# Kernel tuning notes

Hardware: AMD Instinct MI355X
Metric: run time of the kernel (lower is better)

The kernel has to match this reference:

```python
import jax, jax.numpy as jnp
import numpy as np

N_NODES = 10000
N_EDGES = 80000
IN_DIM = 512
H1, H2, OUT_DIM = 4096, 1024, 7
NEG_SLOPE = 0.2


def _gat_layer(x, src, dst, W, a_src, a_dst, b, n_nodes):
    # x: [N, F_in] -> h: [N, F_out]
    h = x @ W
    # per-edge attention logits: a_src . h_i + a_dst . h_j (PyG GATConv, heads=1)
    e = jax.nn.leaky_relu((h @ a_src)[src] + (h @ a_dst)[dst], NEG_SLOPE)
    # segment softmax over destination nodes
    m = jax.ops.segment_max(e, dst, num_segments=n_nodes)
    ex = jnp.exp(e - m[dst])
    denom = jax.ops.segment_sum(ex, dst, num_segments=n_nodes)
    alpha = ex / denom[dst]
    # scatter-add weighted messages
    out = jax.ops.segment_sum(alpha[:, None] * h[src], dst, num_segments=n_nodes)
    return out + b


def setup_inputs() -> dict:
    key = jax.random.key(0)
    ks = jax.random.split(key, 16)
    s = 0.05
    inp = {
        "x": jax.random.normal(ks[0], (N_NODES, IN_DIM), dtype=jnp.float32),
        "edge_index": jax.random.randint(ks[1], (2, N_EDGES), 0, N_NODES, dtype=jnp.int32),
        "W1": jax.random.normal(ks[2], (IN_DIM, H1), dtype=jnp.float32) * s,
        "att_src1": jax.random.normal(ks[3], (H1,), dtype=jnp.float32) * s,
        "att_dst1": jax.random.normal(ks[4], (H1,), dtype=jnp.float32) * s,
        "b1": jnp.zeros((H1,), dtype=jnp.float32),
        "W2": jax.random.normal(ks[5], (H1, H2), dtype=jnp.float32) * s,
        "att_src2": jax.random.normal(ks[6], (H2,), dtype=jnp.float32) * s,
        "att_dst2": jax.random.normal(ks[7], (H2,), dtype=jnp.float32) * s,
        "b2": jnp.zeros((H2,), dtype=jnp.float32),
        "W3": jax.random.normal(ks[8], (H2, OUT_DIM), dtype=jnp.float32) * s,
        "att_src3": jax.random.normal(ks[9], (OUT_DIM,), dtype=jnp.float32) * s,
        "att_dst3": jax.random.normal(ks[10], (OUT_DIM,), dtype=jnp.float32) * s,
        "b3": jnp.zeros((OUT_DIM,), dtype=jnp.float32),
    }
    return inp


def reference(x, edge_index, W1, att_src1, att_dst1, b1,
              W2, att_src2, att_dst2, b2,
              W3, att_src3, att_dst3, b3):
    n = x.shape[0]
    loops = jnp.arange(n, dtype=edge_index.dtype)
    src = jnp.concatenate([edge_index[0], loops])  # add_self_loops=True
    dst = jnp.concatenate([edge_index[1], loops])
    h = _gat_layer(x, src, dst, W1, att_src1, att_dst1, b1, n)
    h = jax.nn.relu(h)  # dropout is identity in eval mode
    h = _gat_layer(h, src, dst, W2, att_src2, att_dst2, b2, n)
    h = jax.nn.relu(h)
    h = _gat_layer(h, src, dst, W3, att_src3, att_dst3, b3, n)
    return jax.nn.log_softmax(h, axis=1)
```

## Files before the change

### kernel.cpp

```cpp
#include <hip/hip_runtime.h>
#include <hip/hip_bf16.h>
#include <math.h>

#define NNODES  10000
#define NEDGES  80000
#define NTOT    90000
#define IN_DIM  512
#define H1_DIM  4096
#define H2_DIM  1024
#define ODIM    7
#define MAXDEG  128
#define NEG_SLOPE 0.2f

typedef __hip_bfloat16 bf16;
typedef __attribute__((ext_vector_type(8))) short short8;
typedef __attribute__((ext_vector_type(4))) float f32x4;

__device__ inline float ldf(const float* p, size_t i) { return p[i]; }
__device__ inline float ldf(const bf16* p, size_t i)  { return __bfloat162float(p[i]); }
__device__ inline void  stf(float* p, size_t i, float v) { p[i] = v; }
__device__ inline void  stf(bf16* p, size_t i, float v)  { p[i] = __float2bfloat16(v); }

#define ASYNC_COPY16(lds, g)                                                              \
    __builtin_amdgcn_global_load_lds((const __attribute__((address_space(1))) void*)(g),  \
                                     (__attribute__((address_space(3))) void*)(lds),      \
                                     16, 0, 0)

__global__ void zero_cnt(int* cnt) {
    int i = blockIdx.x * blockDim.x + threadIdx.x;
    if (i < NNODES) cnt[i] = 0;
}

__global__ void build_bucket(const int* __restrict__ ei, int* cnt, int* bucket) {
    int k = blockIdx.x * blockDim.x + threadIdx.x;
    if (k >= NTOT) return;
    int s, d;
    if (k < NEDGES) { s = ei[k]; d = ei[NEDGES + k]; }
    else            { s = k - NEDGES; d = s; }
    int pos = atomicAdd(&cnt[d], 1);
    if (pos < MAXDEG) bucket[d * MAXDEG + pos] = s;
}

__global__ __launch_bounds__(256) void transpose_bf16(const float* __restrict__ W,
                                                      bf16* __restrict__ WT, int R, int C) {
    __shared__ float t[32][33];
    int c0 = blockIdx.x * 32, r0 = blockIdx.y * 32;
    int x = threadIdx.x & 31, y = threadIdx.x >> 5;
    #pragma unroll
    for (int dy = 0; dy < 32; dy += 8)
        t[y + dy][x] = W[(size_t)(r0 + y + dy) * C + c0 + x];
    __syncthreads();
    #pragma unroll
    for (int dy = 0; dy < 32; dy += 8)
        WT[(size_t)(c0 + y + dy) * R + r0 + x] = __float2bfloat16(t[x][y + dy]);
}

__global__ __launch_bounds__(256) void fold_att(const float* __restrict__ W,
                                                const float* __restrict__ a_s,
                                                const float* __restrict__ a_d,
                                                float* __restrict__ w_s,
                                                float* __restrict__ w_d, int C) {
    int r = blockIdx.x;
    const float* row = W + (size_t)r * C;
    float ss = 0.f, sd = 0.f;
    for (int j = threadIdx.x; j < C; j += 256) {
        float w = row[j];
        ss = fmaf(w, a_s[j], ss);
        sd = fmaf(w, a_d[j], sd);
    }
    #pragma unroll
    for (int off = 32; off > 0; off >>= 1) {
        ss += __shfl_down(ss, off);
        sd += __shfl_down(sd, off);
    }
    __shared__ float red[2][4];
    int wave = threadIdx.x >> 6;
    if ((threadIdx.x & 63) == 0) { red[0][wave] = ss; red[1][wave] = sd; }
    __syncthreads();
    if (threadIdx.x == 0) {
        w_s[r] = red[0][0] + red[0][1] + red[0][2] + red[0][3];
        w_d[r] = red[1][0] + red[1][1] + red[1][2] + red[1][3];
    }
}

template<typename IT>
__global__ __launch_bounds__(256) void node_dots_t(const IT* __restrict__ H,
                                                   const float* __restrict__ w_s,
                                                   const float* __restrict__ w_d,
                                                   float* __restrict__ s_src,
                                                   float* __restrict__ s_dst, int F) {
    int n = blockIdx.x;
    const IT* h = H + (size_t)n * F;
    float ss = 0.f, sd = 0.f;
    for (int f = threadIdx.x; f < F; f += 256) {
        float v = ldf(h, f);
        ss = fmaf(v, w_s[f], ss);
        sd = fmaf(v, w_d[f], sd);
    }
    #pragma unroll
    for (int off = 32; off > 0; off >>= 1) {
        ss += __shfl_down(ss, off);
        sd += __shfl_down(sd, off);
    }
    __shared__ float red[2][4];
    int wave = threadIdx.x >> 6;
    if ((threadIdx.x & 63) == 0) { red[0][wave] = ss; red[1][wave] = sd; }
    __syncthreads();
    if (threadIdx.x == 0) {
        s_src[n] = red[0][0] + red[0][1] + red[0][2] + red[0][3];
        s_dst[n] = red[1][0] + red[1][1] + red[1][2] + red[1][3];
    }
}

template<typename IT, typename OT, bool BIASRELU>
__global__ __launch_bounds__(256) void aggregate_t(const IT* __restrict__ H,
                                                   const float* __restrict__ s_src,
                                                   const float* __restrict__ s_dst,
                                                   const int* __restrict__ bucket,
                                                   const int* __restrict__ cnt,
                                                   const float* __restrict__ bias,
                                                   OT* __restrict__ OUT, int F) {
    int n = blockIdx.x;
    int c = min(cnt[n], MAXDEG);
    __shared__ float alpha[MAXDEG];
    __shared__ int   ssrc[MAXDEG];
    if (threadIdx.x < c) {
        int s = bucket[n * MAXDEG + threadIdx.x];
        ssrc[threadIdx.x] = s;
        float e = s_src[s] + s_dst[n];
        alpha[threadIdx.x] = (e > 0.f) ? e : NEG_SLOPE * e;
    }
    __syncthreads();
    if (threadIdx.x == 0) {
        float m = -1e30f;
        for (int j = 0; j < c; ++j) m = fmaxf(m, alpha[j]);
        float s = 0.f;
        for (int j = 0; j < c; ++j) { float ex = __expf(alpha[j] - m); alpha[j] = ex; s += ex; }
        float inv = 1.f / s;
        for (int j = 0; j < c; ++j) alpha[j] *= inv;
    }
    __syncthreads();
    for (int f = threadIdx.x; f < F; f += 256) {
        float acc = 0.f;
        for (int j = 0; j < c; ++j)
            acc = fmaf(alpha[j], ldf(H, (size_t)ssrc[j] * F + f), acc);
        if (BIASRELU) acc = fmaxf(acc + bias[f], 0.f);
        stf(OUT, (size_t)n * F + f, acc);
    }
}

template<bool BIASRELU>
__global__ __launch_bounds__(256) void gemm_mfma(const bf16* __restrict__ A,
                                                 const bf16* __restrict__ BT,
                                                 const float* __restrict__ bias,
                                                 bf16* __restrict__ C,
                                                 int M, int N, int K) {
    __shared__ alignas(16) bf16 As[128][32];
    __shared__ alignas(16) bf16 Bs[128][32];
    const int tid  = threadIdx.x;
    const int wave = tid >> 6;
    const int lane = tid & 63;
    const int row0 = blockIdx.y * 128;
    const int col0 = blockIdx.x * 128;
    const int wr0  = (wave >> 1) * 64;
    const int wc0  = (wave & 1) * 64;

    const int srow  = tid >> 2;
    const int skoff = (tid & 3) * 8;
    const bf16* ag0 = A  + (size_t)min(row0 + srow,      M - 1) * K + skoff;
    const bf16* ag1 = A  + (size_t)min(row0 + 64 + srow, M - 1) * K + skoff;
    const bf16* bg0 = BT + (size_t)(col0 + srow) * K + skoff;
    const bf16* bg1 = BT + (size_t)(col0 + 64 + srow) * K + skoff;
    bf16* la0 = &As[wave * 16][0];
    bf16* la1 = &As[64 + wave * 16][0];
    bf16* lb0 = &Bs[wave * 16][0];
    bf16* lb1 = &Bs[64 + wave * 16][0];

    f32x4 acc[4][4] = {};

    const int fRow  = lane & 15;
    const int fKoff = (lane >> 4) * 8;

    for (int k0 = 0; k0 < K; k0 += 32) {
        ASYNC_COPY16(la0, ag0);
        ASYNC_COPY16(la1, ag1);
        ASYNC_COPY16(lb0, bg0);
        ASYNC_COPY16(lb1, bg1);
        ag0 += 32; ag1 += 32; bg0 += 32; bg1 += 32;
        __syncthreads();
        short8 af[4], bfr[4];
        #pragma unroll
        for (int i = 0; i < 4; ++i)
            af[i] = *(const short8*)&As[wr0 + i * 16 + fRow][fKoff];
        #pragma unroll
        for (int j = 0; j < 4; ++j)
            bfr[j] = *(const short8*)&Bs[wc0 + j * 16 + fRow][fKoff];
        #pragma unroll
        for (int i = 0; i < 4; ++i)
            #pragma unroll
            for (int j = 0; j < 4; ++j)
                acc[i][j] = __builtin_amdgcn_mfma_f32_16x16x32_bf16(af[i], bfr[j], acc[i][j], 0, 0, 0);
        __syncthreads();
    }

    const int crow = (lane >> 4) * 4;
    const int ccol = lane & 15;
    #pragma unroll
    for (int i = 0; i < 4; ++i) {
        #pragma unroll
        for (int r = 0; r < 4; ++r) {
            int gm = row0 + wr0 + i * 16 + crow + r;
            if (gm < M) {
                #pragma unroll
                for (int j = 0; j < 4; ++j) {
                    int gn = col0 + wc0 + j * 16 + ccol;
                    float v = acc[i][j][r];
                    if (BIASRELU) v = fmaxf(v + bias[gn], 0.f);
                    C[(size_t)gm * N + gn] = __float2bfloat16(v);
                }
            }
        }
    }
}

__global__ __launch_bounds__(256) void layer3_proj(const bf16* __restrict__ X,
                                                   const float* __restrict__ W,
                                                   const float* __restrict__ a_src,
                                                   const float* __restrict__ a_dst,
                                                   float* __restrict__ H3,
                                                   float* __restrict__ s_src,
                                                   float* __restrict__ s_dst) {
    int n = blockIdx.x;
    const bf16* x = X + (size_t)n * H2_DIM;
    float acc[ODIM] = {};
    for (int k = threadIdx.x; k < H2_DIM; k += 256) {
        float xv = __bfloat162float(x[k]);
        #pragma unroll
        for (int o = 0; o < ODIM; ++o)
            acc[o] = fmaf(xv, W[k * ODIM + o], acc[o]);
    }
    #pragma unroll
    for (int o = 0; o < ODIM; ++o)
        #pragma unroll
        for (int off = 32; off > 0; off >>= 1)
            acc[o] += __shfl_down(acc[o], off);
    __shared__ float red[4][ODIM];
    int wave = threadIdx.x >> 6;
    if ((threadIdx.x & 63) == 0)
        for (int o = 0; o < ODIM; ++o) red[wave][o] = acc[o];
    __syncthreads();
    if (threadIdx.x == 0) {
        float ss = 0.f, sd = 0.f;
        for (int o = 0; o < ODIM; ++o) {
            float v = red[0][o] + red[1][o] + red[2][o] + red[3][o];
            H3[n * ODIM + o] = v;
            ss = fmaf(v, a_src[o], ss);
            sd = fmaf(v, a_dst[o], sd);
        }
        s_src[n] = ss; s_dst[n] = sd;
    }
}

__global__ __launch_bounds__(128) void aggregate3(const float* __restrict__ H3,
                                                  const float* __restrict__ s_src,
                                                  const float* __restrict__ s_dst,
                                                  const int* __restrict__ bucket,
                                                  const int* __restrict__ cnt,
                                                  const float* __restrict__ b3,
                                                  float* __restrict__ out) {
    int n = blockIdx.x;
    int c = min(cnt[n], MAXDEG);
    __shared__ float alpha[MAXDEG];
    __shared__ int   ssrc[MAXDEG];
    __shared__ float o[ODIM];
    if (threadIdx.x < c) {
        int s = bucket[n * MAXDEG + threadIdx.x];
        ssrc[threadIdx.x] = s;
        float e = s_src[s] + s_dst[n];
        alpha[threadIdx.x] = (e > 0.f) ? e : NEG_SLOPE * e;
    }
    __syncthreads();
    if (threadIdx.x == 0) {
        float m = -1e30f;
        for (int j = 0; j < c; ++j) m = fmaxf(m, alpha[j]);
        float s = 0.f;
        for (int j = 0; j < c; ++j) { float ex = __expf(alpha[j] - m); alpha[j] = ex; s += ex; }
        float inv = 1.f / s;
        for (int j = 0; j < c; ++j) alpha[j] *= inv;
    }
    __syncthreads();
    if (threadIdx.x < ODIM) {
        float acc = 0.f;
        for (int j = 0; j < c; ++j)
            acc = fmaf(alpha[j], H3[ssrc[j] * ODIM + threadIdx.x], acc);
        o[threadIdx.x] = acc + b3[threadIdx.x];
    }
    __syncthreads();
    if (threadIdx.x == 0) {
        float m = o[0];
        for (int k = 1; k < ODIM; ++k) m = fmaxf(m, o[k]);
        float s = 0.f;
        for (int k = 0; k < ODIM; ++k) s += __expf(o[k] - m);
        float lse = m + logf(s);
        for (int k = 0; k < ODIM; ++k) out[n * ODIM + k] = o[k] - lse;
    }
}

extern "C" void kernel_launch(void* const* d_in, const int* in_sizes, int n_in,
                              void* d_out, int out_size, void* d_ws, size_t ws_size,
                              hipStream_t stream) {
    const float* x   = (const float*)d_in[0];
    const int*   ei  = (const int*)  d_in[1];
    const float* W1  = (const float*)d_in[2];
    const float* as1 = (const float*)d_in[3];
    const float* ad1 = (const float*)d_in[4];
    const float* b1  = (const float*)d_in[5];
    const float* W2  = (const float*)d_in[6];
    const float* as2 = (const float*)d_in[7];
    const float* ad2 = (const float*)d_in[8];
    const float* b2  = (const float*)d_in[9];
    const float* W3  = (const float*)d_in[10];
    const float* as3 = (const float*)d_in[11];
    const float* ad3 = (const float*)d_in[12];
    const float* b3  = (const float*)d_in[13];
    float* outp = (float*)d_out;

    char* p = (char*)d_ws;
    bf16*  x2     = (bf16*)p;   p += (size_t)NNODES * H1_DIM * sizeof(bf16);
    bf16*  r2     = (bf16*)p;   p += (size_t)NNODES * H2_DIM * sizeof(bf16);
    bf16*  r3     = (bf16*)p;   p += (size_t)NNODES * H2_DIM * sizeof(bf16);
    bf16*  W2T    = (bf16*)p;   p += (size_t)H2_DIM * H1_DIM * sizeof(bf16);
    float* h3     = (float*)p;  p += (size_t)NNODES * ODIM * sizeof(float);
    float* ssrc   = (float*)p;  p += NNODES * sizeof(float);
    float* sdst   = (float*)p;  p += NNODES * sizeof(float);
    float* w1s    = (float*)p;  p += IN_DIM * sizeof(float);
    float* w1d    = (float*)p;  p += IN_DIM * sizeof(float);
    float* w2s    = (float*)p;  p += H1_DIM * sizeof(float);
    float* w2d    = (float*)p;  p += H1_DIM * sizeof(float);
    int*   cnt    = (int*)p;    p += NNODES * sizeof(int);
    int*   bucket = (int*)p;    p += (size_t)NNODES * MAXDEG * sizeof(int);
    size_t required = (size_t)(p - (char*)d_ws);
    if (ws_size < required) return;

    bf16* aggxb = r2;
    bf16* h2    = r2;
    bf16* W1T   = r3;
    bf16* x3    = r3;

    zero_cnt<<<(NNODES + 255) / 256, 256, 0, stream>>>(cnt);
    build_bucket<<<(NTOT + 255) / 256, 256, 0, stream>>>(ei, cnt, bucket);

    fold_att<<<IN_DIM, 256, 0, stream>>>(W1, as1, ad1, w1s, w1d, H1_DIM);
    node_dots_t<float><<<NNODES, 256, 0, stream>>>(x, w1s, w1d, ssrc, sdst, IN_DIM);
    aggregate_t<float, bf16, false><<<NNODES, 256, 0, stream>>>(x, ssrc, sdst, bucket, cnt, nullptr, aggxb, IN_DIM);
    {
        dim3 tg(H1_DIM / 32, IN_DIM / 32);
        transpose_bf16<<<tg, 256, 0, stream>>>(W1, W1T, IN_DIM, H1_DIM);
        dim3 g(H1_DIM / 128, (NNODES + 127) / 128);
        gemm_mfma<true><<<g, 256, 0, stream>>>(aggxb, W1T, b1, x2, NNODES, H1_DIM, IN_DIM);
    }

    fold_att<<<H1_DIM, 256, 0, stream>>>(W2, as2, ad2, w2s, w2d, H2_DIM);
    node_dots_t<bf16><<<NNODES, 256, 0, stream>>>(x2, w2s, w2d, ssrc, sdst, H1_DIM);
    {
        dim3 tg(H2_DIM / 32, H1_DIM / 32);
        transpose_bf16<<<tg, 256, 0, stream>>>(W2, W2T, H1_DIM, H2_DIM);
        dim3 g(H2_DIM / 128, (NNODES + 127) / 128);
        gemm_mfma<false><<<g, 256, 0, stream>>>(x2, W2T, nullptr, h2, NNODES, H2_DIM, H1_DIM);
    }
    aggregate_t<bf16, bf16, true><<<NNODES, 256, 0, stream>>>(h2, ssrc, sdst, bucket, cnt, b2, x3, H2_DIM);

    layer3_proj<<<NNODES, 256, 0, stream>>>(x3, W3, as3, ad3, h3, ssrc, sdst);
    aggregate3<<<NNODES, 128, 0, stream>>>(h3, ssrc, sdst, bucket, cnt, b3, outp);
}
```

Before: 499.8 us.

## Fuse layer-2 attention dots into GEMM epilogue, vectorize aggregation, retile GEMM

The layer-2 node dot products move into the layer-1 GEMM epilogue as atomic adds, so the 4096-wide activation is no longer re-read in a separate pass. The aggregation kernels are specialized per layer and use vectorized float4/uint4 loads with 128 threads. The GEMM now stages 64 k-values per barrier and uses a 64-column tile for layer 2 to launch more blocks. The zero-count kernel becomes a memset. Risks: atomics make the dot sums order-dependent, and one 64-wide chunk per barrier raises LDS use.

```diff
diff --git a/kernel.cpp b/kernel.cpp
--- a/kernel.cpp
+++ b/kernel.cpp
@@ -18,18 +18,17 @@
 
 __device__ inline float ldf(const float* p, size_t i) { return p[i]; }
 __device__ inline float ldf(const bf16* p, size_t i)  { return __bfloat162float(p[i]); }
-__device__ inline void  stf(float* p, size_t i, float v) { p[i] = v; }
-__device__ inline void  stf(bf16* p, size_t i, float v)  { p[i] = __float2bfloat16(v); }
+
+__device__ inline void unpack_bf2(unsigned u, float& lo, float& hi) {
+    union { unsigned i; float f; } a, b;
+    a.i = u << 16; b.i = u & 0xffff0000u;
+    lo = a.f; hi = b.f;
+}
 
 #define ASYNC_COPY16(lds, g)                                                              \
     __builtin_amdgcn_global_load_lds((const __attribute__((address_space(1))) void*)(g),  \
                                      (__attribute__((address_space(3))) void*)(lds),      \
                                      16, 0, 0)
-
-__global__ void zero_cnt(int* cnt) {
-    int i = blockIdx.x * blockDim.x + threadIdx.x;
-    if (i < NNODES) cnt[i] = 0;
-}
 
 __global__ void build_bucket(const int* __restrict__ ei, int* cnt, int* bucket) {
     int k = blockIdx.x * blockDim.x + threadIdx.x;
@@ -83,43 +82,39 @@
     }
 }
 
-template<typename IT>
-__global__ __launch_bounds__(256) void node_dots_t(const IT* __restrict__ H,
-                                                   const float* __restrict__ w_s,
-                                                   const float* __restrict__ w_d,
-                                                   float* __restrict__ s_src,
-                                                   float* __restrict__ s_dst, int F) {
+__global__ __launch_bounds__(128) void node_dots1(const float* __restrict__ X,
+                                                  const float* __restrict__ w_s,
+                                                  const float* __restrict__ w_d,
+                                                  float* __restrict__ s_src,
+                                                  float* __restrict__ s_dst) {
     int n = blockIdx.x;
-    const IT* h = H + (size_t)n * F;
-    float ss = 0.f, sd = 0.f;
-    for (int f = threadIdx.x; f < F; f += 256) {
-        float v = ldf(h, f);
-        ss = fmaf(v, w_s[f], ss);
-        sd = fmaf(v, w_d[f], sd);
-    }
+    int t = threadIdx.x;
+    float4 xv = ((const float4*)(X + (size_t)n * IN_DIM))[t];
+    float4 wsv = ((const float4*)w_s)[t];
+    float4 wdv = ((const float4*)w_d)[t];
+    float ss = xv.x*wsv.x + xv.y*wsv.y + xv.z*wsv.z + xv.w*wsv.w;
+    float sd = xv.x*wdv.x + xv.y*wdv.y + xv.z*wdv.z + xv.w*wdv.w;
     #pragma unroll
     for (int off = 32; off > 0; off >>= 1) {
         ss += __shfl_down(ss, off);
         sd += __shfl_down(sd, off);
     }
-    __shared__ float red[2][4];
-    int wave = threadIdx.x >> 6;
-    if ((threadIdx.x & 63) == 0) { red[0][wave] = ss; red[1][wave] = sd; }
-    __syncthreads();
-    if (threadIdx.x == 0) {
-        s_src[n] = red[0][0] + red[0][1] + red[0][2] + red[0][3];
-        s_dst[n] = red[1][0] + red[1][1] + red[1][2] + red[1][3];
-    }
-}
-
-template<typename IT, typename OT, bool BIASRELU>
-__global__ __launch_bounds__(256) void aggregate_t(const IT* __restrict__ H,
-                                                   const float* __restrict__ s_src,
-                                                   const float* __restrict__ s_dst,
-                                                   const int* __restrict__ bucket,
-                                                   const int* __restrict__ cnt,
-                                                   const float* __restrict__ bias,
-                                                   OT* __restrict__ OUT, int F) {
+    __shared__ float red[2][2];
+    int wave = t >> 6;
+    if ((t & 63) == 0) { red[0][wave] = ss; red[1][wave] = sd; }
+    __syncthreads();
+    if (t == 0) {
+        s_src[n] = red[0][0] + red[0][1];
+        s_dst[n] = red[1][0] + red[1][1];
+    }
+}
+
+__global__ __launch_bounds__(128) void agg1(const float* __restrict__ X,
+                                            const float* __restrict__ s_src,
+                                            const float* __restrict__ s_dst,
+                                            const int* __restrict__ bucket,
+                                            const int* __restrict__ cnt,
+                                            bf16* __restrict__ OUT) {
     int n = blockIdx.x;
     int c = min(cnt[n], MAXDEG);
     __shared__ float alpha[MAXDEG];
@@ -140,66 +135,126 @@
         for (int j = 0; j < c; ++j) alpha[j] *= inv;
     }
     __syncthreads();
-    for (int f = threadIdx.x; f < F; f += 256) {
-        float acc = 0.f;
-        for (int j = 0; j < c; ++j)
-            acc = fmaf(alpha[j], ldf(H, (size_t)ssrc[j] * F + f), acc);
-        if (BIASRELU) acc = fmaxf(acc + bias[f], 0.f);
-        stf(OUT, (size_t)n * F + f, acc);
-    }
-}
-
-template<bool BIASRELU>
+    int t = threadIdx.x;
+    float4 acc = {0.f, 0.f, 0.f, 0.f};
+    for (int j = 0; j < c; ++j) {
+        float a = alpha[j];
+        float4 v = ((const float4*)(X + (size_t)ssrc[j] * IN_DIM))[t];
+        acc.x = fmaf(a, v.x, acc.x); acc.y = fmaf(a, v.y, acc.y);
+        acc.z = fmaf(a, v.z, acc.z); acc.w = fmaf(a, v.w, acc.w);
+    }
+    bf16 o[4] = { __float2bfloat16(acc.x), __float2bfloat16(acc.y),
+                  __float2bfloat16(acc.z), __float2bfloat16(acc.w) };
+    *(uint2*)(OUT + (size_t)n * IN_DIM + 4 * t) = *(uint2*)o;
+}
+
+__global__ __launch_bounds__(128) void agg2(const bf16* __restrict__ H,
+                                            const float* __restrict__ s_src,
+                                            const float* __restrict__ s_dst,
+                                            const int* __restrict__ bucket,
+                                            const int* __restrict__ cnt,
+                                            const float* __restrict__ bias,
+                                            bf16* __restrict__ OUT) {
+    int n = blockIdx.x;
+    int c = min(cnt[n], MAXDEG);
+    __shared__ float alpha[MAXDEG];
+    __shared__ int   ssrc[MAXDEG];
+    if (threadIdx.x < c) {
+        int s = bucket[n * MAXDEG + threadIdx.x];
+        ssrc[threadIdx.x] = s;
+        float e = s_src[s] + s_dst[n];
+        alpha[threadIdx.x] = (e > 0.f) ? e : NEG_SLOPE * e;
+    }
+    __syncthreads();
+    if (threadIdx.x == 0) {
+        float m = -1e30f;
+        for (int j = 0; j < c; ++j) m = fmaxf(m, alpha[j]);
+        float s = 0.f;
+        for (int j = 0; j < c; ++j) { float ex = __expf(alpha[j] - m); alpha[j] = ex; s += ex; }
+        float inv = 1.f / s;
+        for (int j = 0; j < c; ++j) alpha[j] *= inv;
+    }
+    __syncthreads();
+    int t = threadIdx.x;
+    float acc[8] = {};
+    for (int j = 0; j < c; ++j) {
+        float a = alpha[j];
+        uint4 raw = ((const uint4*)(H + (size_t)ssrc[j] * H2_DIM))[t];
+        float f0, f1, f2, f3, f4, f5, f6, f7;
+        unpack_bf2(raw.x, f0, f1); unpack_bf2(raw.y, f2, f3);
+        unpack_bf2(raw.z, f4, f5); unpack_bf2(raw.w, f6, f7);
+        acc[0] = fmaf(a, f0, acc[0]); acc[1] = fmaf(a, f1, acc[1]);
+        acc[2] = fmaf(a, f2, acc[2]); acc[3] = fmaf(a, f3, acc[3]);
+        acc[4] = fmaf(a, f4, acc[4]); acc[5] = fmaf(a, f5, acc[5]);
+        acc[6] = fmaf(a, f6, acc[6]); acc[7] = fmaf(a, f7, acc[7]);
+    }
+    bf16 o[8];
+    #pragma unroll
+    for (int k = 0; k < 8; ++k)
+        o[k] = __float2bfloat16(fmaxf(acc[k] + bias[8 * t + k], 0.f));
+    *(uint4*)(OUT + (size_t)n * H2_DIM + 8 * t) = *(uint4*)o;
+}
+
+template<int TN, bool BIASRELU, bool FUSEDOTS>
 __global__ __launch_bounds__(256) void gemm_mfma(const bf16* __restrict__ A,
                                                  const bf16* __restrict__ BT,
                                                  const float* __restrict__ bias,
+                                                 const float* __restrict__ w_s,
+                                                 const float* __restrict__ w_d,
+                                                 float* __restrict__ s_src,
+                                                 float* __restrict__ s_dst,
                                                  bf16* __restrict__ C,
                                                  int M, int N, int K) {
-    __shared__ alignas(16) bf16 As[128][32];
-    __shared__ alignas(16) bf16 Bs[128][32];
+    constexpr int NJ = TN / 32;
+    __shared__ alignas(16) bf16 As[2][128][32];
+    __shared__ alignas(16) bf16 Bs[2][TN][32];
     const int tid  = threadIdx.x;
     const int wave = tid >> 6;
     const int lane = tid & 63;
     const int row0 = blockIdx.y * 128;
-    const int col0 = blockIdx.x * 128;
+    const int col0 = blockIdx.x * TN;
     const int wr0  = (wave >> 1) * 64;
-    const int wc0  = (wave & 1) * 64;
+    const int wc0  = (wave & 1) * (TN / 2);
 
     const int srow  = tid >> 2;
     const int skoff = (tid & 3) * 8;
-    const bf16* ag0 = A  + (size_t)min(row0 + srow,      M - 1) * K + skoff;
-    const bf16* ag1 = A  + (size_t)min(row0 + 64 + srow, M - 1) * K + skoff;
-    const bf16* bg0 = BT + (size_t)(col0 + srow) * K + skoff;
-    const bf16* bg1 = BT + (size_t)(col0 + 64 + srow) * K + skoff;
-    bf16* la0 = &As[wave * 16][0];
-    bf16* la1 = &As[64 + wave * 16][0];
-    bf16* lb0 = &Bs[wave * 16][0];
-    bf16* lb1 = &Bs[64 + wave * 16][0];
-
-    f32x4 acc[4][4] = {};
+    const bf16* agA0 = A + (size_t)min(row0 + srow,      M - 1) * K + skoff;
+    const bf16* agA1 = A + (size_t)min(row0 + 64 + srow, M - 1) * K + skoff;
+    const bf16* bg0  = BT + (size_t)(col0 + srow) * K + skoff;
+    const bf16* bg1  = BT + (size_t)(col0 + (TN == 128 ? 64 : 0) + srow) * K + skoff;
+
+    f32x4 acc[4][NJ] = {};
 
     const int fRow  = lane & 15;
     const int fKoff = (lane >> 4) * 8;
 
-    for (int k0 = 0; k0 < K; k0 += 32) {
-        ASYNC_COPY16(la0, ag0);
-        ASYNC_COPY16(la1, ag1);
-        ASYNC_COPY16(lb0, bg0);
-        ASYNC_COPY16(lb1, bg1);
-        ag0 += 32; ag1 += 32; bg0 += 32; bg1 += 32;
+    for (int k0 = 0; k0 < K; k0 += 64) {
+        #pragma unroll
+        for (int h = 0; h < 2; ++h) {
+            ASYNC_COPY16(&As[h][wave * 16][0],      agA0 + h * 32);
+            ASYNC_COPY16(&As[h][64 + wave * 16][0], agA1 + h * 32);
+            ASYNC_COPY16(&Bs[h][wave * 16][0],      bg0 + h * 32);
+            if constexpr (TN == 128)
+                ASYNC_COPY16(&Bs[h][(TN / 2) + wave * 16][0], bg1 + h * 32);
+        }
+        agA0 += 64; agA1 += 64; bg0 += 64;
+        if constexpr (TN == 128) bg1 += 64;
         __syncthreads();
-        short8 af[4], bfr[4];
-        #pragma unroll
-        for (int i = 0; i < 4; ++i)
-            af[i] = *(const short8*)&As[wr0 + i * 16 + fRow][fKoff];
-        #pragma unroll
-        for (int j = 0; j < 4; ++j)
-            bfr[j] = *(const short8*)&Bs[wc0 + j * 16 + fRow][fKoff];
-        #pragma unroll
-        for (int i = 0; i < 4; ++i)
+        #pragma unroll
+        for (int h = 0; h < 2; ++h) {
+            short8 af[4], bfr[NJ];
             #pragma unroll
-            for (int j = 0; j < 4; ++j)
-                acc[i][j] = __builtin_amdgcn_mfma_f32_16x16x32_bf16(af[i], bfr[j], acc[i][j], 0, 0, 0);
+            for (int i = 0; i < 4; ++i)
+                af[i] = *(const short8*)&As[h][wr0 + i * 16 + fRow][fKoff];
+            #pragma unroll
+            for (int j = 0; j < NJ; ++j)
+                bfr[j] = *(const short8*)&Bs[h][wc0 + j * 16 + fRow][fKoff];
+            #pragma unroll
+            for (int i = 0; i < 4; ++i)
+                #pragma unroll
+                for (int j = 0; j < NJ; ++j)
+                    acc[i][j] = __builtin_amdgcn_mfma_f32_16x16x32_bf16(af[i], bfr[j], acc[i][j], 0, 0, 0);
+        }
         __syncthreads();
     }
 
@@ -210,20 +265,36 @@
         #pragma unroll
         for (int r = 0; r < 4; ++r) {
             int gm = row0 + wr0 + i * 16 + crow + r;
+            float vss = 0.f, vsd = 0.f;
             if (gm < M) {
                 #pragma unroll
-                for (int j = 0; j < 4; ++j) {
+                for (int j = 0; j < NJ; ++j) {
                     int gn = col0 + wc0 + j * 16 + ccol;
                     float v = acc[i][j][r];
                     if (BIASRELU) v = fmaxf(v + bias[gn], 0.f);
                     C[(size_t)gm * N + gn] = __float2bfloat16(v);
+                    if (FUSEDOTS) {
+                        vss = fmaf(v, w_s[gn], vss);
+                        vsd = fmaf(v, w_d[gn], vsd);
+                    }
+                }
+            }
+            if (FUSEDOTS) {
+                #pragma unroll
+                for (int m2 = 1; m2 < 16; m2 <<= 1) {
+                    vss += __shfl_xor(vss, m2, 16);
+                    vsd += __shfl_xor(vsd, m2, 16);
+                }
+                if ((lane & 15) == 0 && gm < M) {
+                    atomicAdd(&s_src[gm], vss);
+                    atomicAdd(&s_dst[gm], vsd);
                 }
             }
         }
     }
 }
 
-__global__ __launch_bounds__(256) void layer3_proj(const bf16* __restrict__ X,
+__global__ __launch_bounds__(128) void layer3_proj(const bf16* __restrict__ X,
                                                    const float* __restrict__ W,
                                                    const float* __restrict__ a_src,
                                                    const float* __restrict__ a_dst,
@@ -231,28 +302,35 @@
                                                    float* __restrict__ s_src,
                                                    float* __restrict__ s_dst) {
     int n = blockIdx.x;
-    const bf16* x = X + (size_t)n * H2_DIM;
+    int t = threadIdx.x;
+    uint4 raw = ((const uint4*)(X + (size_t)n * H2_DIM))[t];
+    float xv[8];
+    unpack_bf2(raw.x, xv[0], xv[1]); unpack_bf2(raw.y, xv[2], xv[3]);
+    unpack_bf2(raw.z, xv[4], xv[5]); unpack_bf2(raw.w, xv[6], xv[7]);
     float acc[ODIM] = {};
-    for (int k = threadIdx.x; k < H2_DIM; k += 256) {
-        float xv = __bfloat162float(x[k]);
+    #pragma unroll
+    for (int e = 0; e < 8; ++e) {
+        const float* wrow = W + (size_t)(8 * t + e) * ODIM;
         #pragma unroll
         for (int o = 0; o < ODIM; ++o)
-            acc[o] = fmaf(xv, W[k * ODIM + o], acc[o]);
+            acc[o] = fmaf(xv[e], wrow[o], acc[o]);
     }
     #pragma unroll
     for (int o = 0; o < ODIM; ++o)
         #pragma unroll
         for (int off = 32; off > 0; off >>= 1)
             acc[o] += __shfl_down(acc[o], off);
-    __shared__ float red[4][ODIM];
-    int wave = threadIdx.x >> 6;
-    if ((threadIdx.x & 63) == 0)
+    __shared__ float red[2][ODIM];
+    int wave = t >> 6;
+    if ((t & 63) == 0)
+        #pragma unroll
         for (int o = 0; o < ODIM; ++o) red[wave][o] = acc[o];
     __syncthreads();
-    if (threadIdx.x == 0) {
+    if (t == 0) {
         float ss = 0.f, sd = 0.f;
+        #pragma unroll
         for (int o = 0; o < ODIM; ++o) {
-            float v = red[0][o] + red[1][o] + red[2][o] + red[3][o];
+            float v = red[0][o] + red[1][o];
             H3[n * ODIM + o] = v;
             ss = fmaf(v, a_src[o], ss);
             sd = fmaf(v, a_dst[o], sd);
@@ -347,29 +425,32 @@
     bf16* W1T   = r3;
     bf16* x3    = r3;
 
-    zero_cnt<<<(NNODES + 255) / 256, 256, 0, stream>>>(cnt);
+    hipMemsetAsync(cnt, 0, NNODES * sizeof(int), stream);
     build_bucket<<<(NTOT + 255) / 256, 256, 0, stream>>>(ei, cnt, bucket);
 
     fold_att<<<IN_DIM, 256, 0, stream>>>(W1, as1, ad1, w1s, w1d, H1_DIM);
-    node_dots_t<float><<<NNODES, 256, 0, stream>>>(x, w1s, w1d, ssrc, sdst, IN_DIM);
-    aggregate_t<float, bf16, false><<<NNODES, 256, 0, stream>>>(x, ssrc, sdst, bucket, cnt, nullptr, aggxb, IN_DIM);
+    node_dots1<<<NNODES, 128, 0, stream>>>(x, w1s, w1d, ssrc, sdst);
+    agg1<<<NNODES, 128, 0, stream>>>(x, ssrc, sdst, bucket, cnt, aggxb);
+
+    fold_att<<<H1_DIM, 256, 0, stream>>>(W2, as2, ad2, w2s, w2d, H2_DIM);
+    hipMemsetAsync(ssrc, 0, 2 * NNODES * sizeof(float), stream);
     {
         dim3 tg(H1_DIM / 32, IN_DIM / 32);
         transpose_bf16<<<tg, 256, 0, stream>>>(W1, W1T, IN_DIM, H1_DIM);
         dim3 g(H1_DIM / 128, (NNODES + 127) / 128);
-        gemm_mfma<true><<<g, 256, 0, stream>>>(aggxb, W1T, b1, x2, NNODES, H1_DIM, IN_DIM);
-    }
-
-    fold_att<<<H1_DIM, 256, 0, stream>>>(W2, as2, ad2, w2s, w2d, H2_DIM);
-    node_dots_t<bf16><<<NNODES, 256, 0, stream>>>(x2, w2s, w2d, ssrc, sdst, H1_DIM);
+        gemm_mfma<128, true, true><<<g, 256, 0, stream>>>(aggxb, W1T, b1, w2s, w2d,
+                                                          ssrc, sdst, x2, NNODES, H1_DIM, IN_DIM);
+    }
+
     {
         dim3 tg(H2_DIM / 32, H1_DIM / 32);
         transpose_bf16<<<tg, 256, 0, stream>>>(W2, W2T, H1_DIM, H2_DIM);
-        dim3 g(H2_DIM / 128, (NNODES + 127) / 128);
-        gemm_mfma<false><<<g, 256, 0, stream>>>(x2, W2T, nullptr, h2, NNODES, H2_DIM, H1_DIM);
-    }
-    aggregate_t<bf16, bf16, true><<<NNODES, 256, 0, stream>>>(h2, ssrc, sdst, bucket, cnt, b2, x3, H2_DIM);
-
-    layer3_proj<<<NNODES, 256, 0, stream>>>(x3, W3, as3, ad3, h3, ssrc, sdst);
+        dim3 g(H2_DIM / 64, (NNODES + 127) / 128);
+        gemm_mfma<64, false, false><<<g, 256, 0, stream>>>(x2, W2T, nullptr, nullptr, nullptr,
+                                                           nullptr, nullptr, h2, NNODES, H2_DIM, H1_DIM);
+    }
+    agg2<<<NNODES, 128, 0, stream>>>(h2, ssrc, sdst, bucket, cnt, b2, x3);
+
+    layer3_proj<<<NNODES, 128, 0, stream>>>(x3, W3, as3, ad3, h3, ssrc, sdst);
     aggregate3<<<NNODES, 128, 0, stream>>>(h3, ssrc, sdst, bucket, cnt, b3, outp);
 }
```

Result: faster. 461.2 us (-7.7%).
